# Kernel tuning notes

Hardware: AMD Instinct MI355X
Metric: run time of the kernel (lower is better)

The kernel has to match this reference:

```python
import jax, jax.numpy as jnp
import numpy as np

VOCAB, EMB, HID, OUT = 10, 32, 64, 10
B, T = 4096, 128

def setup_inputs() -> dict:
    key = jax.random.key(0)
    ks = jax.random.split(key, 8)
    num1 = jax.random.randint(ks[0], (B, T), 0, VOCAB, dtype=jnp.int32)
    num2 = jax.random.randint(ks[1], (B, T), 0, VOCAB, dtype=jnp.int32)
    # Glorot-ish scaled params (values irrelevant for correctness baseline)
    E = jax.random.normal(ks[2], (VOCAB, EMB), jnp.float32) * 0.05
    Wxh = jax.random.normal(ks[3], (2 * EMB, HID), jnp.float32) * (1.0 / np.sqrt(2 * EMB))
    Whh = jax.random.normal(ks[4], (HID, HID), jnp.float32) * (1.0 / np.sqrt(HID))
    b = jax.random.normal(ks[5], (HID,), jnp.float32) * 0.01
    Wd = jax.random.normal(ks[6], (HID, OUT), jnp.float32) * (1.0 / np.sqrt(HID))
    bd = jax.random.normal(ks[7], (OUT,), jnp.float32) * 0.01
    return {"num1": num1, "num2": num2, "E": E, "Wxh": Wxh, "Whh": Whh,
            "b": b, "Wd": Wd, "bd": bd}

def reference(num1, num2, E, Wxh, Whh, b, Wd, bd):
    # Embedding lookup + concat: [B, T, 2*EMB]
    x = jnp.concatenate([E[num1], E[num2]], axis=-1)
    # Precompute input projection for all timesteps (batched GEMM)
    xp = jnp.einsum('bti,ih->bth', x, Wxh) + b  # [B, T, HID]
    h0 = jnp.zeros((x.shape[0], Whh.shape[0]), x.dtype)

    def step(h, xt):  # SimpleRNNCell: h' = tanh(x W_xh + b + h W_hh)
        h = jnp.tanh(xt + h @ Whh)
        return h, h

    _, hs = jax.lax.scan(step, h0, jnp.swapaxes(xp, 0, 1))  # [T, B, HID]
    rnn_out = jnp.swapaxes(hs, 0, 1)  # return_sequences=True -> [B, T, HID]
    logits = rnn_out @ Wd + bd  # [B, T, 10]
    return logits
```

## Files before the change

kernel.cpp:

```cpp
#include <hip/hip_runtime.h>


typedef _Float16 half8 __attribute__((ext_vector_type(8)));
typedef __fp16 fp16x2 __attribute__((ext_vector_type(2)));
typedef float floatx4 __attribute__((ext_vector_type(4)));

#define MFMA16(A, B, C) __builtin_amdgcn_mfma_f32_16x16x32_f16((A), (B), (C), 0, 0, 0)
#define BARRIER() asm volatile("s_waitcnt lgkmcnt(0)\n\ts_barrier" ::: "memory")

#define LUT_DW  17408
#define NP_DW   18432
#define POOL_DW 20512

__global__ __launch_bounds__(256)
void rnn_mfma(const int* __restrict__ num1, const int* __restrict__ num2,
              const float* __restrict__ E, const float* __restrict__ Wxh,
              const float* __restrict__ Whh, const float* __restrict__ bias,
              const float* __restrict__ Wd, const float* __restrict__ bd,
              float* __restrict__ out)
{
    __shared__ __align__(16) int pool[POOL_DW];
    int* lutI  = pool + LUT_DW;
    int* numpk = pool + NP_DW;

    const int tid  = threadIdx.x;
    const int w    = tid >> 6;
    const int lane = tid & 63;
    const int c    = lane & 15;
    const int q    = lane >> 4;
    const int g    = blockIdx.x;

    float* WhhS = (float*)pool;
    float* P1t  = (float*)(pool + 4096);
    float* P2t  = (float*)(pool + 4736);
    float* WdS  = (float*)(pool + 5376);
    for (int i = tid; i < 4096; i += 256) WhhS[i] = Whh[i];
    for (int i = tid; i < 640;  i += 256) WdS[i]  = Wd[i];
    for (int idx = tid; idx < 640; idx += 256) {
        int v = idx >> 6, jj = idx & 63;
        float s1 = bias[jj], s2 = 0.f;
        #pragma unroll
        for (int i = 0; i < 32; ++i) {
            float e = E[v * 32 + i];
            s1 = fmaf(e, Wxh[i * 64 + jj], s1);
            s2 = fmaf(e, Wxh[(32 + i) * 64 + jj], s2);
        }
        P1t[idx] = s1;
        P2t[idx] = s2;
    }
    {
        int e = tid;
        #pragma unroll
        for (int j = 0; j < 4; ++j)
            lutI[e * 4 + j] = (((e >> (2 * j)) & 1) ? 0x3C00 : 0)
                            | (((e >> (2 * j + 1)) & 1) ? 0x3C000000 : 0);
    }
    for (int idx = tid; idx < 2080; idx += 256) {
        int m = idx & 15, t = idx >> 4;
        int s = g * 16 + m;
        numpk[t * 16 + m] = (t < 128)
            ? ((1 << num1[s * 128 + t]) | (1 << (num2[s * 128 + t] + 10))) : 0;
    }
    __syncthreads();

    half8 Wint[4], Wdint[4], Pf;
    #pragma unroll
    for (int kt = 0; kt < 4; ++kt)
        #pragma unroll
        for (int p = 0; p < 4; ++p) {
            int k = kt * 16 + q * 4 + p;
            float wv = WhhS[k * 64 + w * 16 + c];
            Wint[kt][2 * p]     = (_Float16)wv;
            Wint[kt][2 * p + 1] = (_Float16)(wv * 0.015625f);
            float dv = (c < 10) ? WdS[k * 10 + c] : 0.f;
            Wdint[kt][2 * p]     = (_Float16)dv;
            Wdint[kt][2 * p + 1] = (_Float16)(dv * 0.015625f);
        }
    #pragma unroll
    for (int j = 0; j < 8; ++j) {
        int i2 = q * 8 + j;
        float pv = (i2 < 10) ? P1t[i2 * 64 + w * 16 + c]
                 : (i2 < 20) ? P2t[(i2 - 10) * 64 + w * 16 + c] : 0.f;
        Pf[j] = (_Float16)pv;
    }
    float bdv = (c < 10) ? bd[c] : 0.f;
    __syncthreads();

    for (int i = tid; i < 1088; i += 256) pool[15 * 1088 + i] = 0;
    __syncthreads();

    const int rBase = c * 68 + q * 4;
    const int wBase = (q * 4) * 68 + w * 16 + c;

    float* outP[2][4];
    #pragma unroll
    for (int u = 0; u < 2; ++u)
        #pragma unroll
        for (int r = 0; r < 4; ++r)
            outP[u][r] = out + (((g * 16 + q * 4 + r) * 128) + 2 * w + u) * 10 + c;

    const floatx4 zero4 = {0.f, 0.f, 0.f, 0.f};

    floatx4 Cxp;
    {
        int mk = numpk[c];
        int mq = (mk >> (q * 8)) & 0xFF;
        half8 Aoh = *(const half8*)&lutI[mq * 4];
        Cxp = MFMA16(Aoh, Pf, zero4);
    }

    for (int half = 0; half < 16; ++half) {
        const int sb  = (half & 1) * 8;
        const int npo = half * 128 + c;
        #pragma unroll
        for (int i = 0; i < 8; ++i) {
            int mk = numpk[npo + (i + 1) * 16];

            const int spw = sb + i;
            const int spr = (i == 0) ? ((sb ^ 8) + 7) : (sb + i - 1);

            half8 A0 = *(const half8*)&pool[spr * 1088 + rBase];
            half8 A1 = *(const half8*)&pool[spr * 1088 + rBase + 16];
            half8 A2 = *(const half8*)&pool[spr * 1088 + rBase + 32];
            half8 A3 = *(const half8*)&pool[spr * 1088 + rBase + 48];

            floatx4 Ca = MFMA16(A0, Wint[0], Cxp);
            Ca         = MFMA16(A1, Wint[1], Ca);
            floatx4 Cb = MFMA16(A2, Wint[2], zero4);
            Cb         = MFMA16(A3, Wint[3], Cb);

            {
                int mq = (mk >> (q * 8)) & 0xFF;
                half8 Aoh = *(const half8*)&lutI[mq * 4];
                Cxp = MFMA16(Aoh, Pf, zero4);
            }

            float hv[4];
            #pragma unroll
            for (int r = 0; r < 4; ++r) {
                float x  = Ca[r] + Cb[r];
                float e2 = __builtin_amdgcn_exp2f(x * 2.885390081777927f);
                hv[r] = 1.f - 2.f * __builtin_amdgcn_rcpf(e2 + 1.f);
            }
            #pragma unroll
            for (int p = 0; p < 2; ++p) {
                fp16x2 ph = __builtin_amdgcn_cvt_pkrtz(hv[2 * p], hv[2 * p + 1]);
                float c0 = (float)ph[0];
                float c1 = (float)ph[1];
                fp16x2 pl = __builtin_amdgcn_cvt_pkrtz((hv[2 * p] - c0) * 64.f,
                                                       (hv[2 * p + 1] - c1) * 64.f);
                unsigned phu = __builtin_bit_cast(unsigned, ph);
                unsigned plu = __builtin_bit_cast(unsigned, pl);
                unsigned w0 = __builtin_amdgcn_perm(plu, phu, 0x05040100u);
                unsigned w1 = __builtin_amdgcn_perm(plu, phu, 0x07060302u);
                pool[spw * 1088 + wBase + (2 * p) * 68]     = (int)w0;
                pool[spw * 1088 + wBase + (2 * p + 1) * 68] = (int)w1;
            }

            if ((i == 2 || i == 6) && half > 0) {
                const int u   = (i == 6);
                const int sbp = (half & 1) ? 0 : 8;
                const int sl  = (sbp + 2 * w + u) * 1088 + rBase;
                half8 P0 = *(const half8*)&pool[sl];
                half8 P1 = *(const half8*)&pool[sl + 16];
                half8 P2 = *(const half8*)&pool[sl + 32];
                half8 P3 = *(const half8*)&pool[sl + 48];
                floatx4 Cp = MFMA16(P0, Wdint[0], zero4);
                Cp         = MFMA16(P1, Wdint[1], Cp);
                Cp         = MFMA16(P2, Wdint[2], Cp);
                Cp         = MFMA16(P3, Wdint[3], Cp);
                if (c < 10) {
                    #pragma unroll
                    for (int r = 0; r < 4; ++r)
                        outP[u][r][-80] = Cp[r] + bdv;
                }
            }

            BARRIER();
        }
        #pragma unroll
        for (int u = 0; u < 2; ++u)
            #pragma unroll
            for (int r = 0; r < 4; ++r)
                outP[u][r] += 80;
    }

    #pragma unroll
    for (int u = 0; u < 2; ++u) {
        const int sl = (8 + 2 * w + u) * 1088 + rBase;
        half8 P0 = *(const half8*)&pool[sl];
        half8 P1 = *(const half8*)&pool[sl + 16];
        half8 P2 = *(const half8*)&pool[sl + 32];
        half8 P3 = *(const half8*)&pool[sl + 48];
        floatx4 Cp = MFMA16(P0, Wdint[0], zero4);
        Cp         = MFMA16(P1, Wdint[1], Cp);
        Cp         = MFMA16(P2, Wdint[2], Cp);
        Cp         = MFMA16(P3, Wdint[3], Cp);
        if (c < 10) {
            #pragma unroll
            for (int r = 0; r < 4; ++r)
                outP[u][r][-80] = Cp[r] + bdv;
        }
    }
}

extern "C" void kernel_launch(void* const* d_in, const int* in_sizes, int n_in,
                              void* d_out, int out_size, void* d_ws, size_t ws_size,
                              hipStream_t stream) {
    const int*   num1 = (const int*)d_in[0];
    const int*   num2 = (const int*)d_in[1];
    const float* E    = (const float*)d_in[2];
    const float* Wxh  = (const float*)d_in[3];
    const float* Whh  = (const float*)d_in[4];
    const float* b    = (const float*)d_in[5];
    const float* Wd   = (const float*)d_in[6];
    const float* bd   = (const float*)d_in[7];
    float* out = (float*)d_out;
    rnn_mfma<<<256, 256, 0, stream>>>(num1, num2, E, Wxh, Whh, b, Wd, bd, out);
}
```

Before: 119.8 us.

## Shorten RNN step critical path with parallel MFMA chains and prefetched one-hot loads

Splits the four recurrent MFMAs into independent accumulators so they no longer form a dependent chain, and moves the next step's input-projection MFMA after the tanh so it fills the gap. The one-hot LUT read and packed index are prefetched one step ahead, and the LUT is replicated per quad to avoid LDS bank conflicts. The tanh scale 2*log2(e) is folded into Whh and the projection weights, removing one multiply per element. The fp16 hi/lo split now uses a bit mask instead of a convert and convert-back. The cost is more LDS and registers, and a slightly different rounding of the weights.

Measured after the change: 120.0 us. No clear change (+0.2%).

```diff
diff --git a/kernel.cpp b/kernel.cpp
--- a/kernel.cpp
+++ b/kernel.cpp
@@ -7,10 +7,11 @@
 
 #define MFMA16(A, B, C) __builtin_amdgcn_mfma_f32_16x16x32_f16((A), (B), (C), 0, 0, 0)
 #define BARRIER() asm volatile("s_waitcnt lgkmcnt(0)\n\ts_barrier" ::: "memory")
+#define TWO_LOG2E 2.885390081777927f
 
 #define LUT_DW  17408
-#define NP_DW   18432
-#define POOL_DW 20512
+#define NP_DW   21536
+#define POOL_DW 23616
 
 __global__ __launch_bounds__(256)
 void rnn_mfma(const int* __restrict__ num1, const int* __restrict__ num2,
@@ -28,6 +29,7 @@
     const int lane = tid & 63;
     const int c    = lane & 15;
     const int q    = lane >> 4;
+    const int qs   = q * 8;
     const int g    = blockIdx.x;
 
     float* WhhS = (float*)pool;
@@ -51,9 +53,13 @@
     {
         int e = tid;
         #pragma unroll
-        for (int j = 0; j < 4; ++j)
-            lutI[e * 4 + j] = (((e >> (2 * j)) & 1) ? 0x3C00 : 0)
-                            | (((e >> (2 * j + 1)) & 1) ? 0x3C000000 : 0);
+        for (int j = 0; j < 4; ++j) {
+            int v = (((e >> (2 * j)) & 1) ? 0x3C00 : 0)
+                  | (((e >> (2 * j + 1)) & 1) ? 0x3C000000 : 0);
+            #pragma unroll
+            for (int cp = 0; cp < 4; ++cp)
+                lutI[cp * 1032 + e * 4 + j] = v;
+        }
     }
     for (int idx = tid; idx < 2080; idx += 256) {
         int m = idx & 15, t = idx >> 4;
@@ -69,7 +75,7 @@
         #pragma unroll
         for (int p = 0; p < 4; ++p) {
             int k = kt * 16 + q * 4 + p;
-            float wv = WhhS[k * 64 + w * 16 + c];
+            float wv = WhhS[k * 64 + w * 16 + c] * TWO_LOG2E;
             Wint[kt][2 * p]     = (_Float16)wv;
             Wint[kt][2 * p + 1] = (_Float16)(wv * 0.015625f);
             float dv = (c < 10) ? WdS[k * 10 + c] : 0.f;
@@ -78,10 +84,10 @@
         }
     #pragma unroll
     for (int j = 0; j < 8; ++j) {
-        int i2 = q * 8 + j;
+        int i2 = qs + j;
         float pv = (i2 < 10) ? P1t[i2 * 64 + w * 16 + c]
                  : (i2 < 20) ? P2t[(i2 - 10) * 64 + w * 16 + c] : 0.f;
-        Pf[j] = (_Float16)pv;
+        Pf[j] = (_Float16)(pv * TWO_LOG2E);
     }
     float bdv = (c < 10) ? bd[c] : 0.f;
     __syncthreads();
@@ -91,6 +97,7 @@
 
     const int rBase = c * 68 + q * 4;
     const int wBase = (q * 4) * 68 + w * 16 + c;
+    const int lutQ  = q * 1032;
 
     float* outP[2][4];
     #pragma unroll
@@ -103,18 +110,19 @@
 
     floatx4 Cxp;
     {
-        int mk = numpk[c];
-        int mq = (mk >> (q * 8)) & 0xFF;
-        half8 Aoh = *(const half8*)&lutI[mq * 4];
+        int mk0 = numpk[c];
+        half8 Aoh = *(const half8*)&lutI[lutQ + ((mk0 >> qs) & 0xFF) * 4];
         Cxp = MFMA16(Aoh, Pf, zero4);
     }
+    int mkN = numpk[16 + c];
 
     for (int half = 0; half < 16; ++half) {
         const int sb  = (half & 1) * 8;
         const int npo = half * 128 + c;
         #pragma unroll
         for (int i = 0; i < 8; ++i) {
-            int mk = numpk[npo + (i + 1) * 16];
+            half8 Aoh = *(const half8*)&lutI[lutQ + ((mkN >> qs) & 0xFF) * 4];
+            int mkN2 = numpk[npo + (i + 2) * 16];
 
             const int spw = sb + i;
             const int spr = (i == 0) ? ((sb ^ 8) + 7) : (sb + i - 1);
@@ -125,30 +133,26 @@
             half8 A3 = *(const half8*)&pool[spr * 1088 + rBase + 48];
 
             floatx4 Ca = MFMA16(A0, Wint[0], Cxp);
-            Ca         = MFMA16(A1, Wint[1], Ca);
-            floatx4 Cb = MFMA16(A2, Wint[2], zero4);
-            Cb         = MFMA16(A3, Wint[3], Cb);
-
-            {
-                int mq = (mk >> (q * 8)) & 0xFF;
-                half8 Aoh = *(const half8*)&lutI[mq * 4];
-                Cxp = MFMA16(Aoh, Pf, zero4);
-            }
+            floatx4 Cb = MFMA16(A1, Wint[1], zero4);
+            floatx4 Cc = MFMA16(A2, Wint[2], zero4);
+            floatx4 Cd = MFMA16(A3, Wint[3], zero4);
 
             float hv[4];
             #pragma unroll
             for (int r = 0; r < 4; ++r) {
-                float x  = Ca[r] + Cb[r];
-                float e2 = __builtin_amdgcn_exp2f(x * 2.885390081777927f);
+                float x  = (Ca[r] + Cb[r]) + (Cc[r] + Cd[r]);
+                float e2 = __builtin_amdgcn_exp2f(x);
                 hv[r] = 1.f - 2.f * __builtin_amdgcn_rcpf(e2 + 1.f);
             }
             #pragma unroll
             for (int p = 0; p < 2; ++p) {
-                fp16x2 ph = __builtin_amdgcn_cvt_pkrtz(hv[2 * p], hv[2 * p + 1]);
-                float c0 = (float)ph[0];
-                float c1 = (float)ph[1];
-                fp16x2 pl = __builtin_amdgcn_cvt_pkrtz((hv[2 * p] - c0) * 64.f,
-                                                       (hv[2 * p + 1] - c1) * 64.f);
+                unsigned b0 = __builtin_bit_cast(unsigned, hv[2 * p])     & 0xFFFFE000u;
+                unsigned b1 = __builtin_bit_cast(unsigned, hv[2 * p + 1]) & 0xFFFFE000u;
+                float a0 = __builtin_bit_cast(float, b0);
+                float a1 = __builtin_bit_cast(float, b1);
+                fp16x2 ph = __builtin_amdgcn_cvt_pkrtz(a0, a1);
+                fp16x2 pl = __builtin_amdgcn_cvt_pkrtz((hv[2 * p] - a0) * 64.f,
+                                                       (hv[2 * p + 1] - a1) * 64.f);
                 unsigned phu = __builtin_bit_cast(unsigned, ph);
                 unsigned plu = __builtin_bit_cast(unsigned, pl);
                 unsigned w0 = __builtin_amdgcn_perm(plu, phu, 0x05040100u);
@@ -156,6 +160,9 @@
                 pool[spw * 1088 + wBase + (2 * p) * 68]     = (int)w0;
                 pool[spw * 1088 + wBase + (2 * p + 1) * 68] = (int)w1;
             }
+
+            Cxp = MFMA16(Aoh, Pf, zero4);
+            mkN = mkN2;
 
             if ((i == 2 || i == 6) && half > 0) {
                 const int u   = (i == 6);
```

## Specialize 8-step blocks by buffer half and split recurrent MFMA chain

Applied to the files above, without the earlier changes.

Moves the 8-step inner loop into a template specialized on the ping-pong buffer half and on whether the output projection runs. The loop is unrolled by 16 steps, so slot indices become compile-time constants and the half>0 check disappears. The recurrent matmul now uses four independent MFMA accumulators instead of two dependent chains, shortening the serial latency on the critical path. The one-hot index word is prefetched two steps ahead. The trade-off is more code size and higher register pressure.

After: 120.1 us. About the same (+0.2%).

```diff
diff --git a/kernel.cpp b/kernel.cpp
--- a/kernel.cpp
+++ b/kernel.cpp
@@ -11,6 +11,80 @@
 #define LUT_DW  17408
 #define NP_DW   18432
 #define POOL_DW 20512
+
+template <int SB, bool PROJ>
+__device__ __forceinline__ void steps8(
+    int* __restrict__ pool, const int* __restrict__ lutI,
+    const int* __restrict__ npP,
+    const half8 (&Wint)[4], const half8 (&Wdint)[4], const half8& Pf,
+    floatx4& Cxp, int& mkN,
+    const int rBase, const int wBase, const int qs,
+    const int (&projBase)[2], const float bdv, const bool cLt10,
+    float* (&outP)[2][4])
+{
+    const floatx4 zero4 = {0.f, 0.f, 0.f, 0.f};
+    #pragma unroll
+    for (int i = 0; i < 8; ++i) {
+        const int spw = SB + i;
+        const int spr = (i == 0) ? ((SB ^ 8) + 7) : (SB + i - 1);
+
+        half8 A0 = *(const half8*)&pool[spr * 1088 + rBase];
+        half8 A1 = *(const half8*)&pool[spr * 1088 + rBase + 16];
+        half8 A2 = *(const half8*)&pool[spr * 1088 + rBase + 32];
+        half8 A3 = *(const half8*)&pool[spr * 1088 + rBase + 48];
+        half8 Aoh = *(const half8*)&lutI[((mkN >> qs) & 0xFF) * 4];
+        int mkN2 = npP[(i + 2) * 16];
+
+        floatx4 Ca = MFMA16(A0, Wint[0], Cxp);
+        floatx4 Cb = MFMA16(A1, Wint[1], zero4);
+        floatx4 Cc = MFMA16(A2, Wint[2], zero4);
+        floatx4 Cd = MFMA16(A3, Wint[3], zero4);
+        Cxp = MFMA16(Aoh, Pf, zero4);
+        mkN = mkN2;
+
+        float hv[4];
+        #pragma unroll
+        for (int r = 0; r < 4; ++r) {
+            float x  = (Ca[r] + Cb[r]) + (Cc[r] + Cd[r]);
+            float e2 = __builtin_amdgcn_exp2f(x * 2.885390081777927f);
+            hv[r] = 1.f - 2.f * __builtin_amdgcn_rcpf(e2 + 1.f);
+        }
+        #pragma unroll
+        for (int p = 0; p < 2; ++p) {
+            fp16x2 ph = __builtin_amdgcn_cvt_pkrtz(hv[2 * p], hv[2 * p + 1]);
+            float c0 = (float)ph[0];
+            float c1 = (float)ph[1];
+            fp16x2 pl = __builtin_amdgcn_cvt_pkrtz((hv[2 * p] - c0) * 64.f,
+                                                   (hv[2 * p + 1] - c1) * 64.f);
+            unsigned phu = __builtin_bit_cast(unsigned, ph);
+            unsigned plu = __builtin_bit_cast(unsigned, pl);
+            unsigned w0 = __builtin_amdgcn_perm(plu, phu, 0x05040100u);
+            unsigned w1 = __builtin_amdgcn_perm(plu, phu, 0x07060302u);
+            pool[spw * 1088 + wBase + (2 * p) * 68]     = (int)w0;
+            pool[spw * 1088 + wBase + (2 * p + 1) * 68] = (int)w1;
+        }
+
+        if (PROJ && (i == 2 || i == 6)) {
+            const int u = (i == 6) ? 1 : 0;
+            const int sl = projBase[u] + (SB ^ 8) * 1088;
+            half8 P0 = *(const half8*)&pool[sl];
+            half8 P1 = *(const half8*)&pool[sl + 16];
+            half8 P2 = *(const half8*)&pool[sl + 32];
+            half8 P3 = *(const half8*)&pool[sl + 48];
+            floatx4 Cp = MFMA16(P0, Wdint[0], zero4);
+            Cp         = MFMA16(P1, Wdint[1], Cp);
+            Cp         = MFMA16(P2, Wdint[2], Cp);
+            Cp         = MFMA16(P3, Wdint[3], Cp);
+            if (cLt10) {
+                #pragma unroll
+                for (int r = 0; r < 4; ++r)
+                    outP[u][r][-80] = Cp[r] + bdv;
+            }
+        }
+
+        BARRIER();
+    }
+}
 
 __global__ __launch_bounds__(256)
 void rnn_mfma(const int* __restrict__ num1, const int* __restrict__ num2,
@@ -28,6 +102,7 @@
     const int lane = tid & 63;
     const int c    = lane & 15;
     const int q    = lane >> 4;
+    const int qs   = q * 8;
     const int g    = blockIdx.x;
 
     float* WhhS = (float*)pool;
@@ -78,12 +153,13 @@
         }
     #pragma unroll
     for (int j = 0; j < 8; ++j) {
-        int i2 = q * 8 + j;
+        int i2 = qs + j;
         float pv = (i2 < 10) ? P1t[i2 * 64 + w * 16 + c]
                  : (i2 < 20) ? P2t[(i2 - 10) * 64 + w * 16 + c] : 0.f;
         Pf[j] = (_Float16)pv;
     }
     float bdv = (c < 10) ? bd[c] : 0.f;
+    const bool cLt10 = (c < 10);
     __syncthreads();
 
     for (int i = tid; i < 1088; i += 256) pool[15 * 1088 + i] = 0;
@@ -91,6 +167,9 @@
 
     const int rBase = c * 68 + q * 4;
     const int wBase = (q * 4) * 68 + w * 16 + c;
+    int projBase[2];
+    projBase[0] = (2 * w + 0) * 1088 + rBase;
+    projBase[1] = (2 * w + 1) * 1088 + rBase;
 
     float* outP[2][4];
     #pragma unroll
@@ -103,91 +182,37 @@
 
     floatx4 Cxp;
     {
-        int mk = numpk[c];
-        int mq = (mk >> (q * 8)) & 0xFF;
-        half8 Aoh = *(const half8*)&lutI[mq * 4];
+        int mk0 = numpk[c];
+        half8 Aoh = *(const half8*)&lutI[((mk0 >> qs) & 0xFF) * 4];
         Cxp = MFMA16(Aoh, Pf, zero4);
     }
-
-    for (int half = 0; half < 16; ++half) {
-        const int sb  = (half & 1) * 8;
-        const int npo = half * 128 + c;
-        #pragma unroll
-        for (int i = 0; i < 8; ++i) {
-            int mk = numpk[npo + (i + 1) * 16];
-
-            const int spw = sb + i;
-            const int spr = (i == 0) ? ((sb ^ 8) + 7) : (sb + i - 1);
-
-            half8 A0 = *(const half8*)&pool[spr * 1088 + rBase];
-            half8 A1 = *(const half8*)&pool[spr * 1088 + rBase + 16];
-            half8 A2 = *(const half8*)&pool[spr * 1088 + rBase + 32];
-            half8 A3 = *(const half8*)&pool[spr * 1088 + rBase + 48];
-
-            floatx4 Ca = MFMA16(A0, Wint[0], Cxp);
-            Ca         = MFMA16(A1, Wint[1], Ca);
-            floatx4 Cb = MFMA16(A2, Wint[2], zero4);
-            Cb         = MFMA16(A3, Wint[3], Cb);
-
-            {
-                int mq = (mk >> (q * 8)) & 0xFF;
-                half8 Aoh = *(const half8*)&lutI[mq * 4];
-                Cxp = MFMA16(Aoh, Pf, zero4);
-            }
-
-            float hv[4];
-            #pragma unroll
-            for (int r = 0; r < 4; ++r) {
-                float x  = Ca[r] + Cb[r];
-                float e2 = __builtin_amdgcn_exp2f(x * 2.885390081777927f);
-                hv[r] = 1.f - 2.f * __builtin_amdgcn_rcpf(e2 + 1.f);
-            }
-            #pragma unroll
-            for (int p = 0; p < 2; ++p) {
-                fp16x2 ph = __builtin_amdgcn_cvt_pkrtz(hv[2 * p], hv[2 * p + 1]);
-                float c0 = (float)ph[0];
-                float c1 = (float)ph[1];
-                fp16x2 pl = __builtin_amdgcn_cvt_pkrtz((hv[2 * p] - c0) * 64.f,
-                                                       (hv[2 * p + 1] - c1) * 64.f);
-                unsigned phu = __builtin_bit_cast(unsigned, ph);
-                unsigned plu = __builtin_bit_cast(unsigned, pl);
-                unsigned w0 = __builtin_amdgcn_perm(plu, phu, 0x05040100u);
-                unsigned w1 = __builtin_amdgcn_perm(plu, phu, 0x07060302u);
-                pool[spw * 1088 + wBase + (2 * p) * 68]     = (int)w0;
-                pool[spw * 1088 + wBase + (2 * p + 1) * 68] = (int)w1;
-            }
-
-            if ((i == 2 || i == 6) && half > 0) {
-                const int u   = (i == 6);
-                const int sbp = (half & 1) ? 0 : 8;
-                const int sl  = (sbp + 2 * w + u) * 1088 + rBase;
-                half8 P0 = *(const half8*)&pool[sl];
-                half8 P1 = *(const half8*)&pool[sl + 16];
-                half8 P2 = *(const half8*)&pool[sl + 32];
-                half8 P3 = *(const half8*)&pool[sl + 48];
-                floatx4 Cp = MFMA16(P0, Wdint[0], zero4);
-                Cp         = MFMA16(P1, Wdint[1], Cp);
-                Cp         = MFMA16(P2, Wdint[2], Cp);
-                Cp         = MFMA16(P3, Wdint[3], Cp);
-                if (c < 10) {
-                    #pragma unroll
-                    for (int r = 0; r < 4; ++r)
-                        outP[u][r][-80] = Cp[r] + bdv;
-                }
-            }
-
-            BARRIER();
-        }
-        #pragma unroll
-        for (int u = 0; u < 2; ++u)
-            #pragma unroll
-            for (int r = 0; r < 4; ++r)
-                outP[u][r] += 80;
-    }
+    int mkN = numpk[16 + c];
+    const int* npP = numpk + c;
+
+    #define ADV() do { _Pragma("unroll") for (int u_ = 0; u_ < 2; ++u_) \
+        { _Pragma("unroll") for (int r_ = 0; r_ < 4; ++r_) outP[u_][r_] += 80; } } while (0)
+
+    steps8<0, false>(pool, lutI, npP, Wint, Wdint, Pf, Cxp, mkN,
+                     rBase, wBase, qs, projBase, bdv, cLt10, outP);
+    ADV(); npP += 128;
+
+    #pragma unroll 1
+    for (int hh = 0; hh < 7; ++hh) {
+        steps8<8, true>(pool, lutI, npP, Wint, Wdint, Pf, Cxp, mkN,
+                        rBase, wBase, qs, projBase, bdv, cLt10, outP);
+        ADV(); npP += 128;
+        steps8<0, true>(pool, lutI, npP, Wint, Wdint, Pf, Cxp, mkN,
+                        rBase, wBase, qs, projBase, bdv, cLt10, outP);
+        ADV(); npP += 128;
+    }
+    steps8<8, true>(pool, lutI, npP, Wint, Wdint, Pf, Cxp, mkN,
+                    rBase, wBase, qs, projBase, bdv, cLt10, outP);
+    ADV();
+    #undef ADV
 
     #pragma unroll
     for (int u = 0; u < 2; ++u) {
-        const int sl = (8 + 2 * w + u) * 1088 + rBase;
+        const int sl = projBase[u] + 8 * 1088;
         half8 P0 = *(const half8*)&pool[sl];
         half8 P1 = *(const half8*)&pool[sl + 16];
         half8 P2 = *(const half8*)&pool[sl + 32];
@@ -196,7 +221,7 @@
         Cp         = MFMA16(P1, Wdint[1], Cp);
         Cp         = MFMA16(P2, Wdint[2], Cp);
         Cp         = MFMA16(P3, Wdint[3], Cp);
-        if (c < 10) {
+        if (cLt10) {
             #pragma unroll
             for (int r = 0; r < 4; ++r)
                 outP[u][r][-80] = Cp[r] + bdv;
```

## Split output projection onto dedicated consumer warps alongside recurrence warps

Applied to the files above, without the earlier changes.

The block grows to 512 threads. Four producer waves run the serial RNN recurrence, and four consumer waves compute the dense output projection from the shared-memory hidden-state ring, matching the producers barrier for barrier. This takes the periodic Wd MFMA and the global stores off the recurrence's critical path. In exchange, each step's barrier now spans 8 waves, and the consumer waves are mostly idle.

Measured after the change: 115.1 us. 1.04x faster.

```diff
diff --git a/kernel.cpp b/kernel.cpp
--- a/kernel.cpp
+++ b/kernel.cpp
@@ -12,7 +12,7 @@
 #define NP_DW   18432
 #define POOL_DW 20512
 
-__global__ __launch_bounds__(256)
+__global__ __launch_bounds__(512)
 void rnn_mfma(const int* __restrict__ num1, const int* __restrict__ num2,
               const float* __restrict__ E, const float* __restrict__ Wxh,
               const float* __restrict__ Whh, const float* __restrict__ bias,
@@ -24,19 +24,22 @@
     int* numpk = pool + NP_DW;
 
     const int tid  = threadIdx.x;
-    const int w    = tid >> 6;
+    const int wv   = tid >> 6;
+    const bool prod = (wv < 4);
+    const int w    = wv & 3;
     const int lane = tid & 63;
     const int c    = lane & 15;
     const int q    = lane >> 4;
+    const int qs   = q * 8;
     const int g    = blockIdx.x;
 
     float* WhhS = (float*)pool;
     float* P1t  = (float*)(pool + 4096);
     float* P2t  = (float*)(pool + 4736);
     float* WdS  = (float*)(pool + 5376);
-    for (int i = tid; i < 4096; i += 256) WhhS[i] = Whh[i];
-    for (int i = tid; i < 640;  i += 256) WdS[i]  = Wd[i];
-    for (int idx = tid; idx < 640; idx += 256) {
+    for (int i = tid; i < 4096; i += 512) WhhS[i] = Whh[i];
+    for (int i = tid; i < 640;  i += 512) WdS[i]  = Wd[i];
+    for (int idx = tid; idx < 640; idx += 512) {
         int v = idx >> 6, jj = idx & 63;
         float s1 = bias[jj], s2 = 0.f;
         #pragma unroll
@@ -48,14 +51,14 @@
         P1t[idx] = s1;
         P2t[idx] = s2;
     }
-    {
+    if (tid < 256) {
         int e = tid;
         #pragma unroll
         for (int j = 0; j < 4; ++j)
             lutI[e * 4 + j] = (((e >> (2 * j)) & 1) ? 0x3C00 : 0)
                             | (((e >> (2 * j + 1)) & 1) ? 0x3C000000 : 0);
     }
-    for (int idx = tid; idx < 2080; idx += 256) {
+    for (int idx = tid; idx < 2080; idx += 512) {
         int m = idx & 15, t = idx >> 4;
         int s = g * 16 + m;
         numpk[t * 16 + m] = (t < 128)
@@ -64,142 +67,162 @@
     __syncthreads();
 
     half8 Wint[4], Wdint[4], Pf;
-    #pragma unroll
-    for (int kt = 0; kt < 4; ++kt)
-        #pragma unroll
-        for (int p = 0; p < 4; ++p) {
-            int k = kt * 16 + q * 4 + p;
-            float wv = WhhS[k * 64 + w * 16 + c];
-            Wint[kt][2 * p]     = (_Float16)wv;
-            Wint[kt][2 * p + 1] = (_Float16)(wv * 0.015625f);
-            float dv = (c < 10) ? WdS[k * 10 + c] : 0.f;
-            Wdint[kt][2 * p]     = (_Float16)dv;
-            Wdint[kt][2 * p + 1] = (_Float16)(dv * 0.015625f);
-        }
-    #pragma unroll
-    for (int j = 0; j < 8; ++j) {
-        int i2 = q * 8 + j;
-        float pv = (i2 < 10) ? P1t[i2 * 64 + w * 16 + c]
-                 : (i2 < 20) ? P2t[(i2 - 10) * 64 + w * 16 + c] : 0.f;
-        Pf[j] = (_Float16)pv;
-    }
-    float bdv = (c < 10) ? bd[c] : 0.f;
+    float bdv = 0.f;
+    if (prod) {
+        #pragma unroll
+        for (int kt = 0; kt < 4; ++kt)
+            #pragma unroll
+            for (int p = 0; p < 4; ++p) {
+                int k = kt * 16 + q * 4 + p;
+                float wvv = WhhS[k * 64 + w * 16 + c];
+                Wint[kt][2 * p]     = (_Float16)wvv;
+                Wint[kt][2 * p + 1] = (_Float16)(wvv * 0.015625f);
+            }
+        #pragma unroll
+        for (int j = 0; j < 8; ++j) {
+            int i2 = qs + j;
+            float pv = (i2 < 10) ? P1t[i2 * 64 + w * 16 + c]
+                     : (i2 < 20) ? P2t[(i2 - 10) * 64 + w * 16 + c] : 0.f;
+            Pf[j] = (_Float16)pv;
+        }
+    } else {
+        #pragma unroll
+        for (int kt = 0; kt < 4; ++kt)
+            #pragma unroll
+            for (int p = 0; p < 4; ++p) {
+                int k = kt * 16 + q * 4 + p;
+                float dv = (c < 10) ? WdS[k * 10 + c] : 0.f;
+                Wdint[kt][2 * p]     = (_Float16)dv;
+                Wdint[kt][2 * p + 1] = (_Float16)(dv * 0.015625f);
+            }
+        bdv = (c < 10) ? bd[c] : 0.f;
+    }
     __syncthreads();
 
-    for (int i = tid; i < 1088; i += 256) pool[15 * 1088 + i] = 0;
+    for (int i = tid; i < 1088; i += 512) pool[15 * 1088 + i] = 0;
     __syncthreads();
 
     const int rBase = c * 68 + q * 4;
-    const int wBase = (q * 4) * 68 + w * 16 + c;
-
-    float* outP[2][4];
-    #pragma unroll
-    for (int u = 0; u < 2; ++u)
-        #pragma unroll
-        for (int r = 0; r < 4; ++r)
-            outP[u][r] = out + (((g * 16 + q * 4 + r) * 128) + 2 * w + u) * 10 + c;
-
     const floatx4 zero4 = {0.f, 0.f, 0.f, 0.f};
 
-    floatx4 Cxp;
-    {
-        int mk = numpk[c];
-        int mq = (mk >> (q * 8)) & 0xFF;
-        half8 Aoh = *(const half8*)&lutI[mq * 4];
-        Cxp = MFMA16(Aoh, Pf, zero4);
-    }
-
-    for (int half = 0; half < 16; ++half) {
-        const int sb  = (half & 1) * 8;
-        const int npo = half * 128 + c;
-        #pragma unroll
-        for (int i = 0; i < 8; ++i) {
-            int mk = numpk[npo + (i + 1) * 16];
-
-            const int spw = sb + i;
-            const int spr = (i == 0) ? ((sb ^ 8) + 7) : (sb + i - 1);
-
-            half8 A0 = *(const half8*)&pool[spr * 1088 + rBase];
-            half8 A1 = *(const half8*)&pool[spr * 1088 + rBase + 16];
-            half8 A2 = *(const half8*)&pool[spr * 1088 + rBase + 32];
-            half8 A3 = *(const half8*)&pool[spr * 1088 + rBase + 48];
-
-            floatx4 Ca = MFMA16(A0, Wint[0], Cxp);
-            Ca         = MFMA16(A1, Wint[1], Ca);
-            floatx4 Cb = MFMA16(A2, Wint[2], zero4);
-            Cb         = MFMA16(A3, Wint[3], Cb);
-
-            {
-                int mq = (mk >> (q * 8)) & 0xFF;
-                half8 Aoh = *(const half8*)&lutI[mq * 4];
-                Cxp = MFMA16(Aoh, Pf, zero4);
-            }
-
-            float hv[4];
-            #pragma unroll
-            for (int r = 0; r < 4; ++r) {
-                float x  = Ca[r] + Cb[r];
-                float e2 = __builtin_amdgcn_exp2f(x * 2.885390081777927f);
-                hv[r] = 1.f - 2.f * __builtin_amdgcn_rcpf(e2 + 1.f);
-            }
-            #pragma unroll
-            for (int p = 0; p < 2; ++p) {
-                fp16x2 ph = __builtin_amdgcn_cvt_pkrtz(hv[2 * p], hv[2 * p + 1]);
-                float c0 = (float)ph[0];
-                float c1 = (float)ph[1];
-                fp16x2 pl = __builtin_amdgcn_cvt_pkrtz((hv[2 * p] - c0) * 64.f,
-                                                       (hv[2 * p + 1] - c1) * 64.f);
-                unsigned phu = __builtin_bit_cast(unsigned, ph);
-                unsigned plu = __builtin_bit_cast(unsigned, pl);
-                unsigned w0 = __builtin_amdgcn_perm(plu, phu, 0x05040100u);
-                unsigned w1 = __builtin_amdgcn_perm(plu, phu, 0x07060302u);
-                pool[spw * 1088 + wBase + (2 * p) * 68]     = (int)w0;
-                pool[spw * 1088 + wBase + (2 * p + 1) * 68] = (int)w1;
-            }
-
-            if ((i == 2 || i == 6) && half > 0) {
-                const int u   = (i == 6);
-                const int sbp = (half & 1) ? 0 : 8;
-                const int sl  = (sbp + 2 * w + u) * 1088 + rBase;
-                half8 P0 = *(const half8*)&pool[sl];
-                half8 P1 = *(const half8*)&pool[sl + 16];
-                half8 P2 = *(const half8*)&pool[sl + 32];
-                half8 P3 = *(const half8*)&pool[sl + 48];
-                floatx4 Cp = MFMA16(P0, Wdint[0], zero4);
-                Cp         = MFMA16(P1, Wdint[1], Cp);
-                Cp         = MFMA16(P2, Wdint[2], Cp);
-                Cp         = MFMA16(P3, Wdint[3], Cp);
-                if (c < 10) {
+    if (prod) {
+        const int wBase = (q * 4) * 68 + w * 16 + c;
+
+        floatx4 Cxp;
+        {
+            int mk0 = numpk[c];
+            half8 Aoh = *(const half8*)&lutI[((mk0 >> qs) & 0xFF) * 4];
+            Cxp = MFMA16(Aoh, Pf, zero4);
+        }
+
+        for (int half = 0; half < 16; ++half) {
+            const int sb  = (half & 1) * 8;
+            const int npo = half * 128 + c;
+            #pragma unroll
+            for (int i = 0; i < 8; ++i) {
+                int mk = numpk[npo + (i + 1) * 16];
+
+                const int spw = sb + i;
+                const int spr = (i == 0) ? ((sb ^ 8) + 7) : (sb + i - 1);
+
+                half8 A0 = *(const half8*)&pool[spr * 1088 + rBase];
+                half8 A1 = *(const half8*)&pool[spr * 1088 + rBase + 16];
+                half8 A2 = *(const half8*)&pool[spr * 1088 + rBase + 32];
+                half8 A3 = *(const half8*)&pool[spr * 1088 + rBase + 48];
+
+                floatx4 Ca = MFMA16(A0, Wint[0], Cxp);
+                Ca         = MFMA16(A1, Wint[1], Ca);
+                floatx4 Cb = MFMA16(A2, Wint[2], zero4);
+                Cb         = MFMA16(A3, Wint[3], Cb);
+
+                {
+                    int mq = (mk >> qs) & 0xFF;
+                    half8 Aoh = *(const half8*)&lutI[mq * 4];
+                    Cxp = MFMA16(Aoh, Pf, zero4);
+                }
+
+                float hv[4];
+                #pragma unroll
+                for (int r = 0; r < 4; ++r) {
+                    float x  = Ca[r] + Cb[r];
+                    float e2 = __builtin_amdgcn_exp2f(x * 2.885390081777927f);
+                    hv[r] = 1.f - 2.f * __builtin_amdgcn_rcpf(e2 + 1.f);
+                }
+                #pragma unroll
+                for (int p = 0; p < 2; ++p) {
+                    fp16x2 ph = __builtin_amdgcn_cvt_pkrtz(hv[2 * p], hv[2 * p + 1]);
+                    float c0 = (float)ph[0];
+                    float c1 = (float)ph[1];
+                    fp16x2 pl = __builtin_amdgcn_cvt_pkrtz((hv[2 * p] - c0) * 64.f,
+                                                           (hv[2 * p + 1] - c1) * 64.f);
+                    unsigned phu = __builtin_bit_cast(unsigned, ph);
+                    unsigned plu = __builtin_bit_cast(unsigned, pl);
+                    unsigned w0 = __builtin_amdgcn_perm(plu, phu, 0x05040100u);
+                    unsigned w1 = __builtin_amdgcn_perm(plu, phu, 0x07060302u);
+                    pool[spw * 1088 + wBase + (2 * p) * 68]     = (int)w0;
+                    pool[spw * 1088 + wBase + (2 * p + 1) * 68] = (int)w1;
+                }
+
+                BARRIER();
+            }
+        }
+    } else {
+        float* outP[2][4];
+        #pragma unroll
+        for (int u = 0; u < 2; ++u)
+            #pragma unroll
+            for (int r = 0; r < 4; ++r)
+                outP[u][r] = out + (((g * 16 + q * 4 + r) * 128) + 2 * w + u) * 10 + c;
+        const bool cLt10 = (c < 10);
+
+        for (int ph = 0; ph < 16; ++ph) {
+            const int sbp = (ph & 1) ? 0 : 8;
+            #pragma unroll
+            for (int i = 0; i < 8; ++i) {
+                if (ph > 0 && (i == w || i == w + 4)) {
+                    const int u  = (i == w) ? 0 : 1;
+                    const int sl = (sbp + 2 * w + u) * 1088 + rBase;
+                    half8 P0 = *(const half8*)&pool[sl];
+                    half8 P1 = *(const half8*)&pool[sl + 16];
+                    half8 P2 = *(const half8*)&pool[sl + 32];
+                    half8 P3 = *(const half8*)&pool[sl + 48];
+                    floatx4 Cp = MFMA16(P0, Wdint[0], zero4);
+                    Cp         = MFMA16(P1, Wdint[1], Cp);
+                    Cp         = MFMA16(P2, Wdint[2], Cp);
+                    Cp         = MFMA16(P3, Wdint[3], Cp);
+                    if (cLt10) {
+                        #pragma unroll
+                        for (int r = 0; r < 4; ++r)
+                            outP[u][r][0] = Cp[r] + bdv;
+                    }
+                }
+                BARRIER();
+            }
+            if (ph > 0) {
+                #pragma unroll
+                for (int u = 0; u < 2; ++u)
                     #pragma unroll
                     for (int r = 0; r < 4; ++r)
-                        outP[u][r][-80] = Cp[r] + bdv;
-                }
-            }
-
-            BARRIER();
-        }
-        #pragma unroll
-        for (int u = 0; u < 2; ++u)
-            #pragma unroll
-            for (int r = 0; r < 4; ++r)
-                outP[u][r] += 80;
-    }
-
-    #pragma unroll
-    for (int u = 0; u < 2; ++u) {
-        const int sl = (8 + 2 * w + u) * 1088 + rBase;
-        half8 P0 = *(const half8*)&pool[sl];
-        half8 P1 = *(const half8*)&pool[sl + 16];
-        half8 P2 = *(const half8*)&pool[sl + 32];
-        half8 P3 = *(const half8*)&pool[sl + 48];
-        floatx4 Cp = MFMA16(P0, Wdint[0], zero4);
-        Cp         = MFMA16(P1, Wdint[1], Cp);
-        Cp         = MFMA16(P2, Wdint[2], Cp);
-        Cp         = MFMA16(P3, Wdint[3], Cp);
-        if (c < 10) {
-            #pragma unroll
-            for (int r = 0; r < 4; ++r)
-                outP[u][r][-80] = Cp[r] + bdv;
+                        outP[u][r] += 80;
+            }
+        }
+
+        #pragma unroll
+        for (int u = 0; u < 2; ++u) {
+            const int sl = (8 + 2 * w + u) * 1088 + rBase;
+            half8 P0 = *(const half8*)&pool[sl];
+            half8 P1 = *(const half8*)&pool[sl + 16];
+            half8 P2 = *(const half8*)&pool[sl + 32];
+            half8 P3 = *(const half8*)&pool[sl + 48];
+            floatx4 Cp = MFMA16(P0, Wdint[0], zero4);
+            Cp         = MFMA16(P1, Wdint[1], Cp);
+            Cp         = MFMA16(P2, Wdint[2], Cp);
+            Cp         = MFMA16(P3, Wdint[3], Cp);
+            if (cLt10) {
+                #pragma unroll
+                for (int r = 0; r < 4; ++r)
+                    outP[u][r][0] = Cp[r] + bdv;
+            }
         }
     }
 }
@@ -216,5 +239,5 @@
     const float* Wd   = (const float*)d_in[6];
     const float* bd   = (const float*)d_in[7];
     float* out = (float*)d_out;
-    rnn_mfma<<<256, 256, 0, stream>>>(num1, num2, E, Wxh, Whh, b, Wd, bd, out);
+    rnn_mfma<<<256, 512, 0, stream>>>(num1, num2, E, Wxh, Whh, b, Wd, bd, out);
 }
```
